# Kernel optimization log

Hardware: AMD Instinct MI355X
Metric: run time of the kernel (lower is better)

The kernel has to match this reference:

```python
import jax, jax.numpy as jnp
import numpy as np

NA = 131072
DG = 150          # GRU hidden size
DS = 50           # static context dim
DIN = 12          # decoding_steps * 2
VEL_CONST = 0.5


def setup_inputs() -> dict:
    key = jax.random.key(0)
    ks = jax.random.split(key, 18)
    s = 0.1  # weight init scale keeps exp(apd_2) numerically tame
    inp = {
        "z": jax.random.normal(ks[0], (NA, 2), jnp.float32),
        "x_flat": jax.random.normal(ks[1], (NA, DIN), jnp.float32),
        "h": jax.random.normal(ks[2], (1, NA, DG), jnp.float32),
        "static": jax.random.normal(ks[3], (NA, DS), jnp.float32),
        "dx": jax.random.normal(ks[4], (NA, 2), jnp.float32),
        "x_prev": jax.random.normal(ks[5], (NA, 2), jnp.float32),
        # GRU params (torch layout: gates ordered r, z, n; shape [3*DG, in])
        "W_ih": jax.random.normal(ks[6], (3 * DG, DIN), jnp.float32) * s,
        "W_hh": jax.random.normal(ks[7], (3 * DG, DG), jnp.float32) * s,
        "b_ih": jax.random.normal(ks[8], (3 * DG,), jnp.float32) * s,
        "b_hh": jax.random.normal(ks[9], (3 * DG,), jnp.float32) * s,
        # MLP: Linear(200,50) -> Softplus -> Linear(50,50) -> Tanh -> Linear(50,6)
        "W1": jax.random.normal(ks[10], (50, DG + DS), jnp.float32) * s,
        "b1": jax.random.normal(ks[11], (50,), jnp.float32) * s,
        "W2": jax.random.normal(ks[12], (50, 50), jnp.float32) * s,
        "b2": jax.random.normal(ks[13], (50,), jnp.float32) * s,
        "W3": jax.random.normal(ks[14], (6, 50), jnp.float32) * s,
        "b3": jax.random.normal(ks[15], (6,), jnp.float32) * s,
    }
    return inp


def _gru_cell(x, h0, W_ih, W_hh, b_ih, b_hh):
    # torch GRU single step. x: [Na, DIN], h0: [Na, DG]
    gx = x @ W_ih.T + b_ih          # [Na, 3*DG]
    gh = h0 @ W_hh.T + b_hh         # [Na, 3*DG]
    xr, xz, xn = jnp.split(gx, 3, axis=-1)
    hr, hz, hn = jnp.split(gh, 3, axis=-1)
    r = jax.nn.sigmoid(xr + hr)
    zg = jax.nn.sigmoid(xz + hz)
    n = jnp.tanh(xn + r * hn)
    return (1.0 - zg) * n + zg * h0


def reference(z, x_flat, h, static, dx, x_prev,
              W_ih, W_hh, b_ih, b_hh, W1, b1, W2, b2, W3, b3):
    h_new = _gru_cell(x_flat, h[0], W_ih, W_hh, b_ih, b_hh)  # [Na, DG]
    dyn_static = jnp.concatenate([h_new, static], axis=-1)    # [Na, DG+DS]
    hmlp = jax.nn.softplus(dyn_static @ W1.T + b1)
    hmlp = jnp.tanh(hmlp @ W2.T + b2)
    out = hmlp @ W3.T + b3                                    # [Na, 6]

    mu_hat = out[:, :2]
    sh = out[:, 2:].reshape(-1, 2, 2)                         # sigma_hat
    mu = x_prev + VEL_CONST * dx + mu_hat

    b = sh[:, 0, 1] + sh[:, 1, 0]
    apd_2 = sh[:, 0, 0] + sh[:, 1, 1]
    amd_2 = sh[:, 0, 0] - sh[:, 1, 1]
    delta = jnp.sqrt(amd_2 ** 2 + b ** 2)
    sinh = jnp.sinh(delta)
    cosh = jnp.cosh(delta)
    tmp1 = sinh / delta
    tmp2 = amd_2 / tmp1
    s00 = cosh + tmp2
    s01 = b * tmp1
    s11 = cosh - tmp2
    sigma = jnp.stack([jnp.stack([s00, s01], axis=-1),
                       jnp.stack([s01, s11], axis=-1)], axis=-2)  # [Na,2,2]
    sigma = sigma * jnp.exp(apd_2)[:, None, None]

    x = jnp.einsum('nij,nj->ni', sigma, z) + mu
    return x, mu, sigma, h_new[None]
```

## Files before the change

### kernel.cpp

```cpp
#include <hip/hip_runtime.h>
#include <math.h>

#define NA 131072
#define NBLK32 (NA/32)

typedef __bf16 bf16x8 __attribute__((ext_vector_type(8)));
typedef float f32x16 __attribute__((ext_vector_type(16)));

#define APACK_OFF 0
#define BIAS4_OFF 214016
#define W1P_OFF   216448
#define W2P_OFF   243072

__device__ __forceinline__ unsigned short f2b(float f){
  __bf16 h = (__bf16)f;
  unsigned short u;
  __builtin_memcpy(&u, &h, 2);
  return u;
}
__device__ __forceinline__ float b2f(unsigned short u){
  unsigned x = ((unsigned)u) << 16; float f;
  __builtin_memcpy(&f, &x, 4); return f;
}
__device__ __forceinline__ bf16x8 asb(uint4 u){ return __builtin_bit_cast(bf16x8, u); }
__device__ __forceinline__ f32x16 mfma32(bf16x8 a, bf16x8 b, f32x16 c){
  return __builtin_amdgcn_mfma_f32_32x32x16_bf16(a, b, c, 0, 0, 0);
}
__device__ __forceinline__ float fsigmoid(float x){ return 1.f/(1.f+__expf(-x)); }
__device__ __forceinline__ float ftanh(float x){ return 1.f - 2.f/(__expf(2.f*x)+1.f); }

__global__ __launch_bounds__(256) void prep2(
    const float* __restrict__ W_ih, const float* __restrict__ W_hh,
    const float* __restrict__ b_ih, const float* __restrict__ b_hh,
    const float* __restrict__ W1, const float* __restrict__ W2,
    float* __restrict__ ws)
{
  int tid = blockIdx.x*blockDim.x + threadIdx.x;
  int stride = gridDim.x*blockDim.x;
  unsigned short* Ap  = (unsigned short*)((char*)ws + APACK_OFF);
  float*          B4  = (float*)((char*)ws + BIAS4_OFF);
  unsigned short* W1p = (unsigned short*)((char*)ws + W1P_OFF);
  unsigned short* W2p = (unsigned short*)((char*)ws + W2P_OFF);

  for (int s = tid; s < 19*11*64; s += stride){
    int lane = s & 63; int t2 = s >> 6; int ks = t2 % 11; int mt = t2 / 11;
    int R = mt*32 + (lane & 31);
    int kb = ks*16 + (lane >> 5)*8;
    int j = R >> 2, g = R & 3;
    #pragma unroll
    for (int i=0;i<8;i++){
      int k = kb + i; float f = 0.f;
      if (j < 150){
        if (k < 12){
          if (g==0) f = W_ih[j*12+k];
          else if (g==1) f = W_ih[(150+j)*12+k];
          else if (g==3) f = W_ih[(300+j)*12+k];
        } else if (k >= 16 && k < 166){
          int kh = k - 16;
          if (g==0) f = W_hh[j*150+kh];
          else if (g==1) f = W_hh[(150+j)*150+kh];
          else if (g==2) f = W_hh[(300+j)*150+kh];
        }
      }
      Ap[s*8+i] = f2b(f);
    }
  }
  for (int j = tid; j < 152; j += stride){
    float4 bv = make_float4(0.f,0.f,0.f,0.f);
    if (j < 150){
      bv.x = b_ih[j]       + b_hh[j];
      bv.y = b_ih[150+j]   + b_hh[150+j];
      bv.z = b_hh[300+j];
      bv.w = b_ih[300+j];
    }
    ((float4*)B4)[j] = bv;
  }
  for (int s = tid; s < 2*13*64; s += stride){
    int lane = s & 63; int t2 = s >> 6; int ks = t2 % 13; int mt = t2 / 13;
    int o = mt*32 + (lane & 31);
    int kb = ks*16 + (lane >> 5)*8;
    #pragma unroll
    for (int i=0;i<8;i++){
      int k = kb + i;
      float f = (o < 50 && k < 200) ? W1[o*200+k] : 0.f;
      W1p[s*8+i] = f2b(f);
    }
  }
  for (int s = tid; s < 2*4*64; s += stride){
    int lane = s & 63; int t2 = s >> 6; int ks = t2 % 4; int mt = t2 / 4;
    int o = mt*32 + (lane & 31);
    int kb = ks*16 + (lane >> 5)*8;
    #pragma unroll
    for (int i=0;i<8;i++){
      int k = kb + i;
      float f = (o < 50 && k < 50) ? W2[o*50+k] : 0.f;
      W2p[s*8+i] = f2b(f);
    }
  }
}

__global__ __launch_bounds__(256,6) void fused_kernel(
    const float* __restrict__ x_flat, const float* __restrict__ h_in,
    const float* __restrict__ st, const float* __restrict__ z_in,
    const float* __restrict__ dx, const float* __restrict__ xp,
    const float* __restrict__ b1, const float* __restrict__ b2,
    const float* __restrict__ W3, const float* __restrict__ b3,
    const unsigned short* __restrict__ Apack, const float* __restrict__ Bias4,
    const unsigned short* __restrict__ W1p, const unsigned short* __restrict__ W2p,
    float* __restrict__ out)
{
  __shared__ char smem[18432];
  unsigned short* sm_ag = (unsigned short*)smem;
  unsigned short* sm_xf = (unsigned short*)(smem + 13824);
  unsigned short* sm_h1 = (unsigned short*)(smem + 13824);
  float*          sm_h2 = (float*)smem;
  unsigned*       ag32  = (unsigned*)sm_ag;

  int t = threadIdx.x; int lane = t & 63; int w = t >> 6;
  int hi = lane >> 5, cl = lane & 31;
  long ab = (long)blockIdx.x * 32;

  const float2* h2p = (const float2*)h_in;
  for (int s = t; s < 2400; s += 256){
    int a = s/75, k2 = s - a*75;
    float2 v = h2p[ab*75 + s];
    ag32[a*108 + k2] = (unsigned)f2b(v.x) | ((unsigned)f2b(v.y) << 16);
  }
  const float2* s2p = (const float2*)st;
  for (int s = t; s < 800; s += 256){
    int a = s/25, k2 = s - a*25;
    float2 v = s2p[ab*25 + s];
    ag32[a*108 + 75 + k2] = (unsigned)f2b(v.x) | ((unsigned)f2b(v.y) << 16);
  }
  {
    int s = t;
    ag32[(s>>3)*108 + 100 + (s&7)] = 0u;
  }
  for (int s = t; s < 512; s += 256){
    int ln = s >> 3; int i = s & 7;
    int k = ((ln >> 5) << 3) + i;
    int agent = ln & 31;
    unsigned short v = 0;
    if (k < 12) v = f2b(x_flat[(ab+agent)*12 + k]);
    sm_xf[s] = v;
  }
  __syncthreads();

  const uint4* xfv = (const uint4*)sm_xf;
  const uint4* r0v = (const uint4*)(sm_ag + cl*216);
  bf16x8 B0[11];
  B0[0] = asb(xfv[lane]);
  #pragma unroll
  for (int ks=1; ks<11; ks++) B0[ks] = asb(r0v[(ks-1)*2 + hi]);
  __syncthreads();

  for (int s = t; s < 1152; s += 256) ((unsigned*)sm_h1)[s] = 0u;

  const uint4* ApV = (const uint4*)Apack;
  #pragma unroll 1
  for (int mt = w; mt < 19; mt += 4){
    f32x16 acc0;
    #pragma unroll
    for (int q=0;q<4;q++){
      float4 bq = ((const float4*)Bias4)[mt*8 + 2*q + hi];
      acc0[4*q+0]=bq.x; acc0[4*q+1]=bq.y; acc0[4*q+2]=bq.z; acc0[4*q+3]=bq.w;
    }
    const uint4* ap = ApV + (size_t)(mt*11)*64 + lane;
    #pragma unroll
    for (int ks=0; ks<11; ks++){
      acc0 = mfma32(asb(ap[ks*64]), B0[ks], acc0);
    }
    int a = cl;
    #pragma unroll
    for (int q=0;q<4;q++){
      int j = mt*8 + 2*q + hi;
      if (j < 150){
        float h0 = b2f(sm_ag[a*216 + j]);
        float r = fsigmoid(acc0[4*q+0]);
        float z = fsigmoid(acc0[4*q+1]);
        float n = ftanh(acc0[4*q+3] + r*acc0[4*q+2]);
        sm_ag[a*216 + j] = f2b(n + z*(h0 - n));
      }
    }
  }
  __syncthreads();

  float2* oh2 = (float2*)(out + (size_t)8*NA);
  for (int s = t; s < 2400; s += 256){
    unsigned u = ag32[(s/75)*108 + (s - (s/75)*75)];
    float2 v; v.x = b2f((unsigned short)u); v.y = b2f((unsigned short)(u>>16));
    oh2[ab*75 + s] = v;
  }

  if (w < 2){
    int mt2 = w;
    f32x16 acc;
    #pragma unroll
    for (int r=0;r<16;r++){
      int o = mt2*32 + (r&3) + 8*(r>>2) + 4*hi;
      acc[r] = (o < 50) ? b1[o] : 0.f;
    }
    {
      const uint4* rv  = (const uint4*)(sm_ag + cl*216);
      const uint4* w1v = (const uint4*)W1p;
      #pragma unroll
      for (int ks=0; ks<13; ks++){
        acc = mfma32(asb(w1v[(mt2*13+ks)*64 + lane]), asb(rv[ks*2+hi]), acc);
      }
    }
    #pragma unroll
    for (int r=0;r<16;r++){
      int o = mt2*32 + (r&3) + 8*(r>>2) + 4*hi;
      if (o < 50){
        float xx = acc[r];
        float spv = fmaxf(xx,0.f) + __logf(1.f + __expf(-fabsf(xx)));
        sm_h1[cl*72 + o] = f2b(spv);
      }
    }
  }
  __syncthreads();

  if (w < 2){
    int mt2 = w;
    f32x16 acc2;
    #pragma unroll
    for (int r=0;r<16;r++){
      int o = mt2*32 + (r&3) + 8*(r>>2) + 4*hi;
      acc2[r] = (o < 50) ? b2[o] : 0.f;
    }
    {
      const uint4* r1v = (const uint4*)(sm_h1 + cl*72);
      const uint4* w2v = (const uint4*)W2p;
      #pragma unroll
      for (int ks=0; ks<4; ks++){
        acc2 = mfma32(asb(w2v[(mt2*4+ks)*64 + lane]), asb(r1v[ks*2+hi]), acc2);
      }
    }
    #pragma unroll
    for (int r=0;r<16;r++){
      int o = mt2*32 + (r&3) + 8*(r>>2) + 4*hi;
      if (o < 50) sm_h2[cl*51 + o] = ftanh(acc2[r]);
    }
  }
  __syncthreads();

  if (t < 32){
    int a = t; long ga = ab + a;
    float o6[6];
    #pragma unroll
    for (int jj=0;jj<6;jj++) o6[jj] = b3[jj];
    for (int k=0;k<50;k++){
      float v = sm_h2[a*51 + k];
      #pragma unroll
      for (int jj=0;jj<6;jj++) o6[jj] = fmaf(v, W3[jj*50+k], o6[jj]);
    }
    float mu0 = xp[ga*2+0] + 0.5f*dx[ga*2+0] + o6[0];
    float mu1 = xp[ga*2+1] + 0.5f*dx[ga*2+1] + o6[1];
    float bb  = o6[3] + o6[4];
    float apd = o6[2] + o6[5];
    float amd = o6[2] - o6[5];
    float delta = sqrtf(amd*amd + bb*bb);
    float e  = __expf(delta);
    float ei = 1.f/e;
    float sinh_ = 0.5f*(e - ei);
    float cosh_ = 0.5f*(e + ei);
    float tmp1 = sinh_/delta;
    float tmp2 = amd/tmp1;
    float ea = __expf(apd);
    float s00 = (cosh_+tmp2)*ea;
    float s01 = (bb*tmp1)*ea;
    float s11 = (cosh_-tmp2)*ea;
    float z0 = z_in[ga*2+0], z1 = z_in[ga*2+1];
    out[ga*2+0] = s00*z0 + s01*z1 + mu0;
    out[ga*2+1] = s01*z0 + s11*z1 + mu1;
    out[(size_t)2*NA + ga*2+0] = mu0;
    out[(size_t)2*NA + ga*2+1] = mu1;
    out[(size_t)4*NA + ga*4+0] = s00;
    out[(size_t)4*NA + ga*4+1] = s01;
    out[(size_t)4*NA + ga*4+2] = s01;
    out[(size_t)4*NA + ga*4+3] = s11;
  }
}

extern "C" void kernel_launch(void* const* d_in, const int* in_sizes, int n_in,
                              void* d_out, int out_size, void* d_ws, size_t ws_size,
                              hipStream_t stream) {
  const float* z      = (const float*)d_in[0];
  const float* x_flat = (const float*)d_in[1];
  const float* h      = (const float*)d_in[2];
  const float* st     = (const float*)d_in[3];
  const float* dx     = (const float*)d_in[4];
  const float* xp     = (const float*)d_in[5];
  const float* W_ih   = (const float*)d_in[6];
  const float* W_hh   = (const float*)d_in[7];
  const float* b_ih   = (const float*)d_in[8];
  const float* b_hh   = (const float*)d_in[9];
  const float* W1     = (const float*)d_in[10];
  const float* b1     = (const float*)d_in[11];
  const float* W2     = (const float*)d_in[12];
  const float* b2     = (const float*)d_in[13];
  const float* W3     = (const float*)d_in[14];
  const float* b3     = (const float*)d_in[15];
  float* out = (float*)d_out;
  float* ws  = (float*)d_ws;

  const unsigned short* Apack = (const unsigned short*)((char*)ws + APACK_OFF);
  const float*          Bias4 = (const float*)((char*)ws + BIAS4_OFF);
  const unsigned short* W1p   = (const unsigned short*)((char*)ws + W1P_OFF);
  const unsigned short* W2p   = (const unsigned short*)((char*)ws + W2P_OFF);

  hipLaunchKernelGGL(prep2, dim3(128), dim3(256), 0, stream,
                     W_ih, W_hh, b_ih, b_hh, W1, W2, ws);
  hipLaunchKernelGGL(fused_kernel, dim3(NBLK32), dim3(256), 0, stream,
                     x_flat, h, st, z, dx, xp, b1, b2, W3, b3,
                     Apack, Bias4, W1p, W2p, out);
}
```

Baseline: 134.1 us.

## Process 128 agents per block with 512 threads, splitting waves over agent tiles

```diff
diff --git a/kernel.cpp b/kernel.cpp
--- a/kernel.cpp
+++ b/kernel.cpp
@@ -2,7 +2,7 @@
 #include <math.h>
 
 #define NA 131072
-#define NBLK32 (NA/32)
+#define NBLK128 (NA/128)
 
 typedef __bf16 bf16x8 __attribute__((ext_vector_type(8)));
 typedef float f32x16 __attribute__((ext_vector_type(16)));
@@ -99,7 +99,7 @@
   }
 }
 
-__global__ __launch_bounds__(256,6) void fused_kernel(
+__global__ __launch_bounds__(512,4) void fused_kernel(
     const float* __restrict__ x_flat, const float* __restrict__ h_in,
     const float* __restrict__ st, const float* __restrict__ z_in,
     const float* __restrict__ dx, const float* __restrict__ xp,
@@ -109,37 +109,37 @@
     const unsigned short* __restrict__ W1p, const unsigned short* __restrict__ W2p,
     float* __restrict__ out)
 {
-  __shared__ char smem[18432];
+  __shared__ char smem[73728];
   unsigned short* sm_ag = (unsigned short*)smem;
-  unsigned short* sm_xf = (unsigned short*)(smem + 13824);
-  unsigned short* sm_h1 = (unsigned short*)(smem + 13824);
+  unsigned short* sm_xf = (unsigned short*)(smem + 55296);
+  unsigned short* sm_h1 = (unsigned short*)(smem + 55296);
   float*          sm_h2 = (float*)smem;
   unsigned*       ag32  = (unsigned*)sm_ag;
 
   int t = threadIdx.x; int lane = t & 63; int w = t >> 6;
   int hi = lane >> 5, cl = lane & 31;
-  long ab = (long)blockIdx.x * 32;
+  int nt = w & 3;
+  int mlane = w >> 2;
+  long ab = (long)blockIdx.x * 128;
 
   const float2* h2p = (const float2*)h_in;
-  for (int s = t; s < 2400; s += 256){
+  for (int s = t; s < 9600; s += 512){
     int a = s/75, k2 = s - a*75;
     float2 v = h2p[ab*75 + s];
     ag32[a*108 + k2] = (unsigned)f2b(v.x) | ((unsigned)f2b(v.y) << 16);
   }
   const float2* s2p = (const float2*)st;
-  for (int s = t; s < 800; s += 256){
+  for (int s = t; s < 3200; s += 512){
     int a = s/25, k2 = s - a*25;
     float2 v = s2p[ab*25 + s];
     ag32[a*108 + 75 + k2] = (unsigned)f2b(v.x) | ((unsigned)f2b(v.y) << 16);
   }
-  {
-    int s = t;
+  for (int s = t; s < 1024; s += 512)
     ag32[(s>>3)*108 + 100 + (s&7)] = 0u;
-  }
-  for (int s = t; s < 512; s += 256){
-    int ln = s >> 3; int i = s & 7;
+  for (int s = t; s < 2048; s += 512){
+    int nt2 = s >> 9; int r = s & 511; int ln = r >> 3; int i = r & 7;
     int k = ((ln >> 5) << 3) + i;
-    int agent = ln & 31;
+    int agent = nt2*32 + (ln & 31);
     unsigned short v = 0;
     if (k < 12) v = f2b(x_flat[(ab+agent)*12 + k]);
     sm_xf[s] = v;
@@ -147,18 +147,18 @@
   __syncthreads();
 
   const uint4* xfv = (const uint4*)sm_xf;
-  const uint4* r0v = (const uint4*)(sm_ag + cl*216);
+  const uint4* r0v = (const uint4*)(sm_ag + (nt*32 + cl)*216);
   bf16x8 B0[11];
-  B0[0] = asb(xfv[lane]);
+  B0[0] = asb(xfv[nt*64 + lane]);
   #pragma unroll
   for (int ks=1; ks<11; ks++) B0[ks] = asb(r0v[(ks-1)*2 + hi]);
   __syncthreads();
 
-  for (int s = t; s < 1152; s += 256) ((unsigned*)sm_h1)[s] = 0u;
+  for (int s = t; s < 4608; s += 512) ((unsigned*)sm_h1)[s] = 0u;
 
   const uint4* ApV = (const uint4*)Apack;
   #pragma unroll 1
-  for (int mt = w; mt < 19; mt += 4){
+  for (int mt = mlane; mt < 19; mt += 2){
     f32x16 acc0;
     #pragma unroll
     for (int q=0;q<4;q++){
@@ -170,7 +170,7 @@
     for (int ks=0; ks<11; ks++){
       acc0 = mfma32(asb(ap[ks*64]), B0[ks], acc0);
     }
-    int a = cl;
+    int a = nt*32 + cl;
     #pragma unroll
     for (int q=0;q<4;q++){
       int j = mt*8 + 2*q + hi;
@@ -186,14 +186,14 @@
   __syncthreads();
 
   float2* oh2 = (float2*)(out + (size_t)8*NA);
-  for (int s = t; s < 2400; s += 256){
+  for (int s = t; s < 9600; s += 512){
     unsigned u = ag32[(s/75)*108 + (s - (s/75)*75)];
     float2 v; v.x = b2f((unsigned short)u); v.y = b2f((unsigned short)(u>>16));
     oh2[ab*75 + s] = v;
   }
 
-  if (w < 2){
-    int mt2 = w;
+  int mt2 = mlane; int a2 = nt*32 + cl;
+  {
     f32x16 acc;
     #pragma unroll
     for (int r=0;r<16;r++){
@@ -201,7 +201,7 @@
       acc[r] = (o < 50) ? b1[o] : 0.f;
     }
     {
-      const uint4* rv  = (const uint4*)(sm_ag + cl*216);
+      const uint4* rv  = (const uint4*)(sm_ag + a2*216);
       const uint4* w1v = (const uint4*)W1p;
       #pragma unroll
       for (int ks=0; ks<13; ks++){
@@ -214,14 +214,13 @@
       if (o < 50){
         float xx = acc[r];
         float spv = fmaxf(xx,0.f) + __logf(1.f + __expf(-fabsf(xx)));
-        sm_h1[cl*72 + o] = f2b(spv);
-      }
-    }
-  }
-  __syncthreads();
-
-  if (w < 2){
-    int mt2 = w;
+        sm_h1[a2*72 + o] = f2b(spv);
+      }
+    }
+  }
+  __syncthreads();
+
+  {
     f32x16 acc2;
     #pragma unroll
     for (int r=0;r<16;r++){
@@ -229,7 +228,7 @@
       acc2[r] = (o < 50) ? b2[o] : 0.f;
     }
     {
-      const uint4* r1v = (const uint4*)(sm_h1 + cl*72);
+      const uint4* r1v = (const uint4*)(sm_h1 + a2*72);
       const uint4* w2v = (const uint4*)W2p;
       #pragma unroll
       for (int ks=0; ks<4; ks++){
@@ -239,12 +238,12 @@
     #pragma unroll
     for (int r=0;r<16;r++){
       int o = mt2*32 + (r&3) + 8*(r>>2) + 4*hi;
-      if (o < 50) sm_h2[cl*51 + o] = ftanh(acc2[r]);
-    }
-  }
-  __syncthreads();
-
-  if (t < 32){
+      if (o < 50) sm_h2[a2*51 + o] = ftanh(acc2[r]);
+    }
+  }
+  __syncthreads();
+
+  if (t < 128){
     int a = t; long ga = ab + a;
     float o6[6];
     #pragma unroll
@@ -311,7 +310,7 @@
 
   hipLaunchKernelGGL(prep2, dim3(128), dim3(256), 0, stream,
                      W_ih, W_hh, b_ih, b_hh, W1, W2, ws);
-  hipLaunchKernelGGL(fused_kernel, dim3(NBLK32), dim3(256), 0, stream,
+  hipLaunchKernelGGL(fused_kernel, dim3(NBLK128), dim3(512), 0, stream,
                      x_flat, h, st, z, dx, xp, b1, b2, W3, b3,
                      Apack, Bias4, W1p, W2p, out);
 }
```

Measured after the change: 110.8 us. -17.4%, faster.
